# Performance work log

Measured on AMD Instinct MI355X. Metric: run time of the kernel, lower is better.

## Reference

```python
import jax, jax.numpy as jnp
import numpy as np

N, S, SKV, K, V = 16, 4096, 4096, 64, 64


def setup_inputs() -> dict:
    key = jax.random.key(0)
    k1, k2, k3, k4 = jax.random.split(key, 4)
    return {
        "queries": jax.random.normal(k1, (N, S, K), dtype=jnp.float32),
        "keys": jax.random.normal(k2, (N, SKV, K), dtype=jnp.float32),
        "values": jax.random.normal(k3, (N, SKV, V), dtype=jnp.float32),
        "mask": jax.random.normal(k4, (S, SKV), dtype=jnp.float32),
    }


def reference(queries, keys, values, mask):
    # queries scaled by K^{-1/2}, then baddbmm(mask, q, k^T)
    scale = queries.shape[-1] ** -0.5
    q = queries * scale
    # scores: [N, S, SKV]; mask (S, SKV) broadcasts over batch like baddbmm
    scores = jnp.einsum('nsk,ntk->nst', q, keys) + mask
    attn_weights = jax.nn.softmax(scores, axis=-1)
    # attn: [N, S, V]; dropout_p = 0.0 (eval), needs_weights = False
    attn = jnp.einsum('nst,ntv->nsv', attn_weights, values)
    return attn
```

## Files before the change

### kernel.cpp

```cpp
#include <hip/hip_runtime.h>
#include <cstdint>
#include <cstddef>


typedef __attribute__((ext_vector_type(8))) short short8;
typedef __attribute__((ext_vector_type(4))) short short4v;
typedef __attribute__((ext_vector_type(4))) float f32x4;
typedef __attribute__((ext_vector_type(4))) unsigned int uint4v;
typedef __attribute__((ext_vector_type(2))) unsigned int uint2v;

#define DEV __device__ __forceinline__

constexpr int N_B   = 16;
constexpr int S_Q   = 4096;
constexpr int S_KV  = 4096;
constexpr int DH    = 64;
constexpr int BQ    = 128;
constexpr int BK    = 64;
constexpr int ITERS = S_KV / BK;
constexpr int KSTR  = 72;
constexpr int VSTR  = 68;
constexpr int KIMG_B = 9216;
constexpr int VIMG_B = 9216;
constexpr int TILE_B = KIMG_B + VIMG_B;

#define LOG2E 1.44269504088896340736f
#define QSCALE (0.125f * 1.44269504088896340736f)

DEV unsigned short f2bf(float f) {
  union { float f; unsigned int i; } x; x.f = f;
  unsigned int r = x.i + 0x7FFFu + ((x.i >> 16) & 1u);
  return (unsigned short)(r >> 16);
}

#if __has_builtin(__builtin_amdgcn_cvt_pk_bf16_f32)
typedef __attribute__((ext_vector_type(2))) __bf16 bf16x2v;
DEV unsigned int packrne(float a, float b) {
  union { bf16x2v v; unsigned int u; } x;
  x.v = __builtin_amdgcn_cvt_pk_bf16_f32(a, b);
  return x.u;
}
#else
DEV unsigned int packrne(float a, float b) {
  union { float f; unsigned int u; } ua, ub; ua.f = a; ub.f = b;
  unsigned int ra = ua.u + 0x7FFFu + ((ua.u >> 16) & 1u);
  unsigned int rb = ub.u + 0x7FFFu + ((ub.u >> 16) & 1u);
  return __builtin_amdgcn_perm(rb, ra, 0x07060302u);
}
#endif

DEV f32x4 mfma16(short4v a, short4v b, f32x4 c) {
#if __has_builtin(__builtin_amdgcn_mfma_f32_16x16x16bf16_1k)
  return __builtin_amdgcn_mfma_f32_16x16x16bf16_1k(a, b, c, 0, 0, 0);
#elif __has_builtin(__builtin_amdgcn_mfma_f32_16x16x16_bf16)
  return __builtin_amdgcn_mfma_f32_16x16x16_bf16(a, b, c, 0, 0, 0);
#else
  asm volatile("v_mfma_f32_16x16x16_bf16 %0, %1, %2, %0\n\ts_nop 7\n\ts_nop 7"
               : "+v"(c) : "v"(a), "v"(b));
  return c;
#endif
}

DEV void stageK(unsigned short* buf, const f32x4* L, int tS) {
  const int r0 = tS >> 3, c = tS & 7;
  uint4v d0, d1;
  d0[0] = packrne(L[0][0], L[0][1]); d0[1] = packrne(L[0][2], L[0][3]);
  d0[2] = packrne(L[1][0], L[1][1]); d0[3] = packrne(L[1][2], L[1][3]);
  d1[0] = packrne(L[2][0], L[2][1]); d1[1] = packrne(L[2][2], L[2][3]);
  d1[2] = packrne(L[3][0], L[3][1]); d1[3] = packrne(L[3][2], L[3][3]);
  *(uint4v*)&buf[r0 * KSTR + c * 8]        = d0;
  *(uint4v*)&buf[(r0 + 32) * KSTR + c * 8] = d1;
}

DEV void stageV(unsigned short* buf, const f32x4* L, int tS) {
  const int a = tS >> 4;
  const int x = tS & 15;
  const int slot = (a + x) & 15;
#pragma unroll
  for (int j = 0; j < 4; ++j) {
    uint2v d;
    d[0] = packrne(L[0][j], L[1][j]);
    d[1] = packrne(L[2][j], L[3][j]);
    *(uint2v*)&buf[(x * 4 + j) * VSTR + slot * 4] = d;
  }
}

DEV void dma16(const void* g, void* l) {
#if __has_builtin(__builtin_amdgcn_global_load_lds)
  __builtin_amdgcn_global_load_lds(
      (const __attribute__((address_space(1))) unsigned int*)g,
      (__attribute__((address_space(3))) unsigned int*)l, 16, 0, 0);
#else
  ((uint4v*)l)[threadIdx.x & 63] = *(const uint4v*)g;
#endif
}

DEV void dmaTile(const char* gt, void* lk, void* lv, int w, int laneB) {
  if (w < 4) {
    const int base = w * 2048;
    dma16(gt + base + laneB,        (char*)lk + base);
    dma16(gt + base + 1024 + laneB, (char*)lk + base + 1024);
    if (w == 0) dma16(gt + 8192 + laneB, (char*)lk + 8192);
  } else {
    const char* g = gt + KIMG_B;
    const int base = (w - 4) * 2048;
    dma16(g + base + laneB,        (char*)lv + base);
    dma16(g + base + 1024 + laneB, (char*)lv + base + 1024);
    if (w == 4) dma16(g + 8192 + laneB, (char*)lv + 8192);
  }
}

__global__ __launch_bounds__(256)
void sdpa_prep(const float* __restrict__ Kg, const float* __restrict__ Vg,
               unsigned short* __restrict__ imgs) {
  const int b   = blockIdx.x;
  const int n   = b >> 6, tau = b & 63;
  const int tS  = threadIdx.x;
  unsigned short* img = imgs + (size_t)b * (TILE_B / 2);
  {
    const float* kp =
        Kg + ((size_t)n * S_KV + tau * 64 + (tS >> 3)) * DH + (tS & 7) * 8;
    f32x4 L[4];
    L[0] = *(const f32x4*)(kp);
    L[1] = *(const f32x4*)(kp + 4);
    L[2] = *(const f32x4*)(kp + 32 * DH);
    L[3] = *(const f32x4*)(kp + 32 * DH + 4);
    stageK(img, L, tS);
  }
  {
    const float* vp =
        Vg + ((size_t)n * S_KV + tau * 64 + (size_t)(tS >> 4) * 4) * DH
           + (tS & 15) * 4;
    f32x4 L[4];
#pragma unroll
    for (int i = 0; i < 4; ++i) L[i] = *(const f32x4*)(vp + i * DH);
    stageV(img + KIMG_B / 2, L, tS);
  }
}

template <int MW>
__global__ __launch_bounds__(512, MW)
void sdpa_fwd_dma(const float* __restrict__ Qg,
                  const float* __restrict__ Mg,
                  const unsigned short* __restrict__ imgs,
                  float* __restrict__ Ob,
                  float* __restrict__ Lb,
                  int nIter)
{
  __shared__ __align__(16) unsigned short ldsK[2][KIMG_B / 2];
  __shared__ __align__(16) unsigned short ldsV[2][VIMG_B / 2];

  const int n     = blockIdx.y;
  const int q0    = blockIdx.x * BQ;
  const int z     = blockIdx.z;
  const int t     = threadIdx.x;
  const int w     = t >> 6;
  const int lane  = t & 63;
  const int l15   = lane & 15;
  const int quad  = lane >> 4;
  const int qrow  = q0 + w * 16 + l15;
  const int laneB = lane * 16;
  const int tbase = n * 64 + z * nIter;

  short8 qf0, qf1;
  {
    const float* qp = Qg + ((size_t)n * S_Q + (size_t)qrow) * DH + quad * 8;
#pragma unroll
    for (int j = 0; j < 8; ++j) {
      qf0[j] = (short)f2bf(qp[j] * QSCALE);
      qf1[j] = (short)f2bf(qp[32 + j] * QSCALE);
    }
  }

  const float* mrow =
      Mg + (size_t)qrow * S_KV + (size_t)z * nIter * BK + quad * 4;

  f32x4 acc[4];
#pragma unroll
  for (int nt = 0; nt < 4; ++nt)
#pragma unroll
    for (int r = 0; r < 4; ++r) acc[nt][r] = 0.0f;
  float rs = 0.0f;

  dmaTile((const char*)imgs + (size_t)tbase * TILE_B,
          &ldsK[0][0], &ldsV[0][0], w, laneB);
  __syncthreads();

  for (int it = 0; it < nIter; ++it) {
    const int p   = it & 1;
    const int kv0 = it * BK;
    const bool more = (it + 1 < nIter);

    if (more)
      dmaTile((const char*)imgs + (size_t)(tbase + it + 1) * TILE_B,
              &ldsK[p ^ 1][0], &ldsV[p ^ 1][0], w, laneB);

    short4v pf[4];
#pragma unroll
    for (int h = 0; h < 4; ++h) {
      const short8 kf0 =
          *(const short8*)&ldsK[p][(l15 + 16 * h) * KSTR + quad * 8];
      const short8 kf1 =
          *(const short8*)&ldsK[p][(l15 + 16 * h) * KSTR + (quad + 4) * 8];
      const f32x4 mk = *(const f32x4*)(mrow + kv0 + 16 * h);
      f32x4 c = {0.f, 0.f, 0.f, 0.f};
      __builtin_amdgcn_s_setprio(1);
      c = __builtin_amdgcn_mfma_f32_16x16x32_bf16(kf0, qf0, c, 0, 0, 0);
      c = __builtin_amdgcn_mfma_f32_16x16x32_bf16(kf1, qf1, c, 0, 0, 0);
      __builtin_amdgcn_s_setprio(0);
      float e[4];
#pragma unroll
      for (int r = 0; r < 4; ++r)
        e[r] = __builtin_amdgcn_exp2f(fmaf(mk[r], LOG2E, c[r]));
      rs += (e[0] + e[1]) + (e[2] + e[3]);
      union { uint2v u; short4v s; } ue;
      ue.u[0] = packrne(e[0], e[1]);
      ue.u[1] = packrne(e[2], e[3]);
      pf[h] = ue.s;
    }

    __builtin_amdgcn_s_setprio(1);
#pragma unroll
    for (int nt = 0; nt < 4; ++nt) {
      const int vcol = l15 + 16 * nt;
      const int xr   = (l15 >> 2) + 4 * nt;
#pragma unroll
      for (int h = 0; h < 4; ++h) {
        const int slot = ((4 * h + quad) + xr) & 15;
        short4v vf = *(const short4v*)&ldsV[p][vcol * VSTR + slot * 4];
        acc[nt] = mfma16(vf, pf[h], acc[nt]);
      }
    }
    __builtin_amdgcn_s_setprio(0);

    __syncthreads();
  }

  rs += __shfl_xor(rs, 16, 64);
  rs += __shfl_xor(rs, 32, 64);

  if (Lb) {
    const size_t NSV = (size_t)N_B * S_Q * DH;
    float* ob = Ob + (size_t)z * NSV + ((size_t)n * S_Q + (size_t)qrow) * DH
              + quad * 4;
#pragma unroll
    for (int nt = 0; nt < 4; ++nt) *(f32x4*)(ob + 16 * nt) = acc[nt];
    if (quad == 0) {
      float* lp = Lb + (size_t)z * ((size_t)N_B * S_Q) + (size_t)n * S_Q
                + (size_t)qrow;
      lp[0] = rs;
    }
  } else {
    const float inv = 1.0f / rs;
    float* ob = Ob + ((size_t)n * S_Q + (size_t)qrow) * DH + quad * 4;
#pragma unroll
    for (int nt = 0; nt < 4; ++nt) {
      f32x4 o;
#pragma unroll
      for (int r = 0; r < 4; ++r) o[r] = acc[nt][r] * inv;
      *(f32x4*)(ob + 16 * nt) = o;
    }
  }
}

__global__ __launch_bounds__(512, 4)
void sdpa_fwd_reg(const float* __restrict__ Qg, const float* __restrict__ Kg,
                  const float* __restrict__ Vg, const float* __restrict__ Mg,
                  float* __restrict__ Og)
{
  __shared__ __align__(16) unsigned short ldsK[2][BK * KSTR];
  __shared__ __align__(16) unsigned short ldsV[2][DH * VSTR];

  const int n = blockIdx.y, q0 = blockIdx.x * BQ, t = threadIdx.x;
  const int w = t >> 6, lane = t & 63, l15 = lane & 15, quad = lane >> 4;
  const int qrow = q0 + w * 16 + l15;

  short8 qf0, qf1;
  {
    const float* qp = Qg + ((size_t)n * S_Q + (size_t)qrow) * DH + quad * 8;
#pragma unroll
    for (int j = 0; j < 8; ++j) {
      qf0[j] = (short)f2bf(qp[j] * QSCALE);
      qf1[j] = (short)f2bf(qp[32 + j] * QSCALE);
    }
  }
  const bool isK = (w < 4);
  const int  tS  = t & 255;
  const float* sgp =
      isK ? Kg + ((size_t)n * S_KV + (size_t)(tS >> 3)) * DH + (tS & 7) * 8
          : Vg + ((size_t)n * S_KV + (size_t)(tS >> 4) * 4) * DH + (tS & 15) * 4;
  const float* mrow = Mg + (size_t)qrow * S_KV + quad * 4;

  f32x4 acc[4];
#pragma unroll
  for (int nt = 0; nt < 4; ++nt)
#pragma unroll
    for (int r = 0; r < 4; ++r) acc[nt][r] = 0.0f;
  float rs = 0.0f;

  {
    f32x4 L[4];
    if (isK) {
      L[0] = *(const f32x4*)(sgp);
      L[1] = *(const f32x4*)(sgp + 4);
      L[2] = *(const f32x4*)(sgp + 32 * DH);
      L[3] = *(const f32x4*)(sgp + 32 * DH + 4);
      stageK(&ldsK[0][0], L, tS);
    } else {
#pragma unroll
      for (int i = 0; i < 4; ++i) L[i] = *(const f32x4*)(sgp + i * DH);
      stageV(&ldsV[0][0], L, tS);
    }
  }
  __syncthreads();

  for (int it = 0; it < ITERS; ++it) {
    const int p = it & 1, kv0 = it * BK;
    const bool more = (it + 1 < ITERS);
    short4v pf[4];
#pragma unroll
    for (int h = 0; h < 4; ++h) {
      const short8 kf0 =
          *(const short8*)&ldsK[p][(l15 + 16 * h) * KSTR + quad * 8];
      const short8 kf1 =
          *(const short8*)&ldsK[p][(l15 + 16 * h) * KSTR + (quad + 4) * 8];
      const f32x4 mk = *(const f32x4*)(mrow + kv0 + 16 * h);
      f32x4 c = {0.f, 0.f, 0.f, 0.f};
      c = __builtin_amdgcn_mfma_f32_16x16x32_bf16(kf0, qf0, c, 0, 0, 0);
      c = __builtin_amdgcn_mfma_f32_16x16x32_bf16(kf1, qf1, c, 0, 0, 0);
      float e[4];
#pragma unroll
      for (int r = 0; r < 4; ++r)
        e[r] = __builtin_amdgcn_exp2f(fmaf(mk[r], LOG2E, c[r]));
      rs += (e[0] + e[1]) + (e[2] + e[3]);
      union { uint2v u; short4v s; } ue;
      ue.u[0] = packrne(e[0], e[1]);
      ue.u[1] = packrne(e[2], e[3]);
      pf[h] = ue.s;
    }
    f32x4 L[4];
    if (more) {
      const float* np = sgp + (size_t)(kv0 + BK) * DH;
      if (isK) {
        L[0] = *(const f32x4*)(np);
        L[1] = *(const f32x4*)(np + 4);
        L[2] = *(const f32x4*)(np + 32 * DH);
        L[3] = *(const f32x4*)(np + 32 * DH + 4);
      } else {
#pragma unroll
        for (int i = 0; i < 4; ++i) L[i] = *(const f32x4*)(np + i * DH);
      }
    }
#pragma unroll
    for (int nt = 0; nt < 4; ++nt) {
      const int vcol = l15 + 16 * nt;
      const int xr   = (l15 >> 2) + 4 * nt;
#pragma unroll
      for (int h = 0; h < 4; ++h) {
        const int slot = ((4 * h + quad) + xr) & 15;
        short4v vf = *(const short4v*)&ldsV[p][vcol * VSTR + slot * 4];
        acc[nt] = mfma16(vf, pf[h], acc[nt]);
      }
    }
    if (more) {
      if (isK) stageK(&ldsK[p ^ 1][0], L, tS);
      else     stageV(&ldsV[p ^ 1][0], L, tS);
    }
    __syncthreads();
  }

  rs += __shfl_xor(rs, 16, 64);
  rs += __shfl_xor(rs, 32, 64);
  const float inv = 1.0f / rs;
  float* ob = Og + ((size_t)n * S_Q + (size_t)qrow) * DH + quad * 4;
#pragma unroll
  for (int nt = 0; nt < 4; ++nt) {
    f32x4 o;
#pragma unroll
    for (int r = 0; r < 4; ++r) o[r] = acc[nt][r] * inv;
    *(f32x4*)(ob + 16 * nt) = o;
  }
}

__global__ __launch_bounds__(256)
void sdpa_combine(const float* __restrict__ ws, float* __restrict__ Og) {
  constexpr size_t NSV = (size_t)N_B * S_Q * DH;
  constexpr size_t NS  = (size_t)N_B * S_Q;
  const size_t i = (size_t)blockIdx.x * 256 + threadIdx.x;
  const f32x4* A0 = (const f32x4*)ws;
  const f32x4* A1 = A0 + NSV / 4;
  const float* L0 = ws + 2 * NSV;
  const float* L1 = L0 + NS;
  const size_t qi = i >> 4;
  const f32x4 a = A0[i], b = A1[i];
  const float inv = 1.0f / (L0[qi] + L1[qi]);
  f32x4 o;
#pragma unroll
  for (int r = 0; r < 4; ++r) o[r] = (a[r] + b[r]) * inv;
  ((f32x4*)Og)[i] = o;
}

extern "C" void kernel_launch(void* const* d_in, const int* in_sizes, int n_in,
                              void* d_out, int out_size, void* d_ws, size_t ws_size,
                              hipStream_t stream) {
  (void)in_sizes; (void)n_in; (void)out_size;
  const float* q = (const float*)d_in[0];
  const float* k = (const float*)d_in[1];
  const float* v = (const float*)d_in[2];
  const float* m = (const float*)d_in[3];
  float* o = (float*)d_out;

  constexpr size_t NSV = (size_t)N_B * S_Q * DH;
  constexpr size_t NS  = (size_t)N_B * S_Q;
  constexpr size_t IMG_BYTES = (size_t)N_B * 64 * TILE_B;
  constexpr size_t SPL_BYTES = (2 * NSV + 2 * NS) * sizeof(float);

  static int use8 = -1;
  if (use8 < 0) {
    hipFuncAttributes attr{};
    use8 = 0;
    if (hipFuncGetAttributes(&attr,
            reinterpret_cast<const void*>(&sdpa_fwd_dma<8>)) == hipSuccess &&
        attr.localSizeBytes == 0)
      use8 = 1;
  }

  if (d_ws != nullptr && ws_size >= IMG_BYTES + SPL_BYTES && use8) {
    unsigned short* imgs = (unsigned short*)d_ws;
    float* part = (float*)((char*)d_ws + IMG_BYTES);
    hipLaunchKernelGGL(sdpa_prep, dim3(N_B * 64), dim3(256), 0, stream,
                       k, v, imgs);
    dim3 grid(S_Q / BQ, N_B, 2);
    hipLaunchKernelGGL((sdpa_fwd_dma<8>), grid, dim3(512), 0, stream,
                       q, m, imgs, part, part + 2 * NSV, ITERS / 2);
    hipLaunchKernelGGL(sdpa_combine, dim3((unsigned)(NSV / 4 / 256)),
                       dim3(256), 0, stream, (const float*)part, o);
  } else if (d_ws != nullptr && ws_size >= IMG_BYTES) {
    unsigned short* imgs = (unsigned short*)d_ws;
    hipLaunchKernelGGL(sdpa_prep, dim3(N_B * 64), dim3(256), 0, stream,
                       k, v, imgs);
    dim3 grid(S_Q / BQ, N_B, 1);
    hipLaunchKernelGGL((sdpa_fwd_dma<4>), grid, dim3(512), 0, stream,
                       q, m, imgs, o, (float*)nullptr, ITERS);
  } else {
    dim3 grid(S_Q / BQ, N_B);
    hipLaunchKernelGGL(sdpa_fwd_reg, grid, dim3(512), 0, stream,
                       q, k, v, m, o);
  }
}
```

Before: 295.7 us.

## Process two query tiles per wave and merge KV splits with atomics

Adds a dual-tile forward kernel in which each of 4 waves handles 32 query rows (two 16-row MFMA tiles), so every K and V fragment read from LDS is reused twice and the block shrinks to 256 threads. The two KV-split halves are now accumulated directly into the output and a row-sum buffer with float atomics, after a zero-fill kernel, and a normalize kernel runs last. This replaces the partial-result workspace and the combine kernel. In exchange it doubles register pressure per wave, issues many scalar global atomics, and adds a zeroing pass over the output.

New measurement: 296.6 us. About the same (+0.3%).

```diff
diff --git a/kernel.cpp b/kernel.cpp
--- a/kernel.cpp
+++ b/kernel.cpp
@@ -107,6 +107,17 @@
     dma16(g + base + laneB,        (char*)lv + base);
     dma16(g + base + 1024 + laneB, (char*)lv + base + 1024);
     if (w == 4) dma16(g + 8192 + laneB, (char*)lv + 8192);
+  }
+}
+
+DEV void dmaTile4(const char* gt, char* lk, char* lv, int w, int laneB) {
+#pragma unroll
+  for (int i = 0; i < 5; ++i) {
+    const int c = w + 4 * i;
+    if (c < 18) {
+      if (c < 9) dma16(gt + c * 1024 + laneB, lk + c * 1024);
+      else dma16(gt + KIMG_B + (c - 9) * 1024 + laneB, lv + (c - 9) * 1024);
+    }
   }
 }
 
@@ -139,13 +150,13 @@
 }
 
 template <int MW>
-__global__ __launch_bounds__(512, MW)
-void sdpa_fwd_dma(const float* __restrict__ Qg,
-                  const float* __restrict__ Mg,
-                  const unsigned short* __restrict__ imgs,
-                  float* __restrict__ Ob,
-                  float* __restrict__ Lb,
-                  int nIter)
+__global__ __launch_bounds__(256, MW)
+void sdpa_fwd_dual(const float* __restrict__ Qg,
+                   const float* __restrict__ Mg,
+                   const unsigned short* __restrict__ imgs,
+                   float* __restrict__ Og,
+                   float* __restrict__ Lbuf,
+                   int nIter)
 {
   __shared__ __align__(16) unsigned short ldsK[2][KIMG_B / 2];
   __shared__ __align__(16) unsigned short ldsV[2][VIMG_B / 2];
@@ -158,9 +169,153 @@
   const int lane  = t & 63;
   const int l15   = lane & 15;
   const int quad  = lane >> 4;
+  const int qA    = q0 + w * 32 + l15;
+  const int laneB = lane * 16;
+  const int tbase = n * 64 + z * nIter;
+
+  short8 qfA0, qfA1, qfB0, qfB1;
+  {
+    const float* qp = Qg + ((size_t)n * S_Q + (size_t)qA) * DH + quad * 8;
+#pragma unroll
+    for (int j = 0; j < 8; ++j) {
+      qfA0[j] = (short)f2bf(qp[j] * QSCALE);
+      qfA1[j] = (short)f2bf(qp[32 + j] * QSCALE);
+      qfB0[j] = (short)f2bf(qp[16 * DH + j] * QSCALE);
+      qfB1[j] = (short)f2bf(qp[16 * DH + 32 + j] * QSCALE);
+    }
+  }
+
+  const float* mrowA =
+      Mg + (size_t)qA * S_KV + (size_t)z * nIter * BK + quad * 4;
+  const float* mrowB = mrowA + (size_t)16 * S_KV;
+
+  f32x4 accA[4], accB[4];
+#pragma unroll
+  for (int nt = 0; nt < 4; ++nt)
+#pragma unroll
+    for (int r = 0; r < 4; ++r) { accA[nt][r] = 0.0f; accB[nt][r] = 0.0f; }
+  float rsA = 0.0f, rsB = 0.0f;
+
+  dmaTile4((const char*)imgs + (size_t)tbase * TILE_B,
+           (char*)&ldsK[0][0], (char*)&ldsV[0][0], w, laneB);
+  __syncthreads();
+
+  for (int it = 0; it < nIter; ++it) {
+    const int p   = it & 1;
+    const int kv0 = it * BK;
+    const bool more = (it + 1 < nIter);
+
+    if (more)
+      dmaTile4((const char*)imgs + (size_t)(tbase + it + 1) * TILE_B,
+               (char*)&ldsK[p ^ 1][0], (char*)&ldsV[p ^ 1][0], w, laneB);
+
+    short4v pfA[4], pfB[4];
+#pragma unroll
+    for (int h = 0; h < 4; ++h) {
+      const short8 kf0 =
+          *(const short8*)&ldsK[p][(l15 + 16 * h) * KSTR + quad * 8];
+      const short8 kf1 =
+          *(const short8*)&ldsK[p][(l15 + 16 * h) * KSTR + (quad + 4) * 8];
+      const f32x4 mkA = *(const f32x4*)(mrowA + kv0 + 16 * h);
+      const f32x4 mkB = *(const f32x4*)(mrowB + kv0 + 16 * h);
+      f32x4 cA = {0.f, 0.f, 0.f, 0.f}, cB = {0.f, 0.f, 0.f, 0.f};
+      __builtin_amdgcn_s_setprio(1);
+      cA = __builtin_amdgcn_mfma_f32_16x16x32_bf16(kf0, qfA0, cA, 0, 0, 0);
+      cB = __builtin_amdgcn_mfma_f32_16x16x32_bf16(kf0, qfB0, cB, 0, 0, 0);
+      cA = __builtin_amdgcn_mfma_f32_16x16x32_bf16(kf1, qfA1, cA, 0, 0, 0);
+      cB = __builtin_amdgcn_mfma_f32_16x16x32_bf16(kf1, qfB1, cB, 0, 0, 0);
+      __builtin_amdgcn_s_setprio(0);
+      float eA[4], eB[4];
+#pragma unroll
+      for (int r = 0; r < 4; ++r) {
+        eA[r] = __builtin_amdgcn_exp2f(fmaf(mkA[r], LOG2E, cA[r]));
+        eB[r] = __builtin_amdgcn_exp2f(fmaf(mkB[r], LOG2E, cB[r]));
+      }
+      rsA += (eA[0] + eA[1]) + (eA[2] + eA[3]);
+      rsB += (eB[0] + eB[1]) + (eB[2] + eB[3]);
+      union { uint2v u; short4v s; } ua, ub;
+      ua.u[0] = packrne(eA[0], eA[1]); ua.u[1] = packrne(eA[2], eA[3]);
+      ub.u[0] = packrne(eB[0], eB[1]); ub.u[1] = packrne(eB[2], eB[3]);
+      pfA[h] = ua.s; pfB[h] = ub.s;
+    }
+
+    __builtin_amdgcn_s_setprio(1);
+#pragma unroll
+    for (int nt = 0; nt < 4; ++nt) {
+      const int vcol = l15 + 16 * nt;
+      const int xr   = (l15 >> 2) + 4 * nt;
+#pragma unroll
+      for (int h = 0; h < 4; ++h) {
+        const int slot = ((4 * h + quad) + xr) & 15;
+        short4v vf = *(const short4v*)&ldsV[p][vcol * VSTR + slot * 4];
+        accA[nt] = mfma16(vf, pfA[h], accA[nt]);
+        accB[nt] = mfma16(vf, pfB[h], accB[nt]);
+      }
+    }
+    __builtin_amdgcn_s_setprio(0);
+
+    __syncthreads();
+  }
+
+  rsA += __shfl_xor(rsA, 16, 64);
+  rsA += __shfl_xor(rsA, 32, 64);
+  rsB += __shfl_xor(rsB, 16, 64);
+  rsB += __shfl_xor(rsB, 32, 64);
+  if (quad == 0) {
+    atomicAdd(&Lbuf[(size_t)n * S_Q + qA],      rsA);
+    atomicAdd(&Lbuf[(size_t)n * S_Q + qA + 16], rsB);
+  }
+  float* obA = Og + ((size_t)n * S_Q + (size_t)qA) * DH + quad * 4;
+  float* obB = obA + (size_t)16 * DH;
+#pragma unroll
+  for (int nt = 0; nt < 4; ++nt)
+#pragma unroll
+    for (int r = 0; r < 4; ++r) {
+      atomicAdd(obA + 16 * nt + r, accA[nt][r]);
+      atomicAdd(obB + 16 * nt + r, accB[nt][r]);
+    }
+}
+
+__global__ __launch_bounds__(256)
+void sdpa_zero(float* __restrict__ Og, float* __restrict__ Lbuf) {
+  constexpr size_t NS = (size_t)N_B * S_Q;
+  const size_t i = (size_t)blockIdx.x * 256 + threadIdx.x;
+  const f32x4 zz = {0.f, 0.f, 0.f, 0.f};
+  ((f32x4*)Og)[i] = zz;
+  if (i < NS / 4) ((f32x4*)Lbuf)[i] = zz;
+}
+
+__global__ __launch_bounds__(256)
+void sdpa_norm(float* __restrict__ Og, const float* __restrict__ Lbuf) {
+  const size_t i = (size_t)blockIdx.x * 256 + threadIdx.x;
+  const size_t qi = i >> 4;
+  f32x4 v = ((f32x4*)Og)[i];
+  const float inv = 1.0f / Lbuf[qi];
+#pragma unroll
+  for (int r = 0; r < 4; ++r) v[r] *= inv;
+  ((f32x4*)Og)[i] = v;
+}
+
+template <int MW>
+__global__ __launch_bounds__(512, MW)
+void sdpa_fwd_dma(const float* __restrict__ Qg,
+                  const float* __restrict__ Mg,
+                  const unsigned short* __restrict__ imgs,
+                  float* __restrict__ Og, int nIter)
+{
+  __shared__ __align__(16) unsigned short ldsK[2][KIMG_B / 2];
+  __shared__ __align__(16) unsigned short ldsV[2][VIMG_B / 2];
+
+  const int n     = blockIdx.y;
+  const int q0    = blockIdx.x * BQ;
+  const int t     = threadIdx.x;
+  const int w     = t >> 6;
+  const int lane  = t & 63;
+  const int l15   = lane & 15;
+  const int quad  = lane >> 4;
   const int qrow  = q0 + w * 16 + l15;
   const int laneB = lane * 16;
-  const int tbase = n * 64 + z * nIter;
+  const int tbase = n * 64;
 
   short8 qf0, qf1;
   {
@@ -171,9 +326,7 @@
       qf1[j] = (short)f2bf(qp[32 + j] * QSCALE);
     }
   }
-
-  const float* mrow =
-      Mg + (size_t)qrow * S_KV + (size_t)z * nIter * BK + quad * 4;
+  const float* mrow = Mg + (size_t)qrow * S_KV + quad * 4;
 
   f32x4 acc[4];
 #pragma unroll
@@ -238,28 +391,14 @@
 
   rs += __shfl_xor(rs, 16, 64);
   rs += __shfl_xor(rs, 32, 64);
-
-  if (Lb) {
-    const size_t NSV = (size_t)N_B * S_Q * DH;
-    float* ob = Ob + (size_t)z * NSV + ((size_t)n * S_Q + (size_t)qrow) * DH
-              + quad * 4;
-#pragma unroll
-    for (int nt = 0; nt < 4; ++nt) *(f32x4*)(ob + 16 * nt) = acc[nt];
-    if (quad == 0) {
-      float* lp = Lb + (size_t)z * ((size_t)N_B * S_Q) + (size_t)n * S_Q
-                + (size_t)qrow;
-      lp[0] = rs;
-    }
-  } else {
-    const float inv = 1.0f / rs;
-    float* ob = Ob + ((size_t)n * S_Q + (size_t)qrow) * DH + quad * 4;
-#pragma unroll
-    for (int nt = 0; nt < 4; ++nt) {
-      f32x4 o;
-#pragma unroll
-      for (int r = 0; r < 4; ++r) o[r] = acc[nt][r] * inv;
-      *(f32x4*)(ob + 16 * nt) = o;
-    }
+  const float inv = 1.0f / rs;
+  float* ob = Og + ((size_t)n * S_Q + (size_t)qrow) * DH + quad * 4;
+#pragma unroll
+  for (int nt = 0; nt < 4; ++nt) {
+    f32x4 o;
+#pragma unroll
+    for (int r = 0; r < 4; ++r) o[r] = acc[nt][r] * inv;
+    *(f32x4*)(ob + 16 * nt) = o;
   }
 }
 
@@ -382,24 +521,6 @@
   }
 }
 
-__global__ __launch_bounds__(256)
-void sdpa_combine(const float* __restrict__ ws, float* __restrict__ Og) {
-  constexpr size_t NSV = (size_t)N_B * S_Q * DH;
-  constexpr size_t NS  = (size_t)N_B * S_Q;
-  const size_t i = (size_t)blockIdx.x * 256 + threadIdx.x;
-  const f32x4* A0 = (const f32x4*)ws;
-  const f32x4* A1 = A0 + NSV / 4;
-  const float* L0 = ws + 2 * NSV;
-  const float* L1 = L0 + NS;
-  const size_t qi = i >> 4;
-  const f32x4 a = A0[i], b = A1[i];
-  const float inv = 1.0f / (L0[qi] + L1[qi]);
-  f32x4 o;
-#pragma unroll
-  for (int r = 0; r < 4; ++r) o[r] = (a[r] + b[r]) * inv;
-  ((f32x4*)Og)[i] = o;
-}
-
 extern "C" void kernel_launch(void* const* d_in, const int* in_sizes, int n_in,
                               void* d_out, int out_size, void* d_ws, size_t ws_size,
                               hipStream_t stream) {
@@ -413,35 +534,37 @@
   constexpr size_t NSV = (size_t)N_B * S_Q * DH;
   constexpr size_t NS  = (size_t)N_B * S_Q;
   constexpr size_t IMG_BYTES = (size_t)N_B * 64 * TILE_B;
-  constexpr size_t SPL_BYTES = (2 * NSV + 2 * NS) * sizeof(float);
-
-  static int use8 = -1;
-  if (use8 < 0) {
+  constexpr size_t DUAL_NEED = IMG_BYTES + NS * sizeof(float);
+
+  static int useDual = -1;
+  if (useDual < 0) {
     hipFuncAttributes attr{};
-    use8 = 0;
+    useDual = 0;
     if (hipFuncGetAttributes(&attr,
-            reinterpret_cast<const void*>(&sdpa_fwd_dma<8>)) == hipSuccess &&
+            reinterpret_cast<const void*>(&sdpa_fwd_dual<4>)) == hipSuccess &&
         attr.localSizeBytes == 0)
-      use8 = 1;
-  }
-
-  if (d_ws != nullptr && ws_size >= IMG_BYTES + SPL_BYTES && use8) {
+      useDual = 1;
+  }
+
+  if (d_ws != nullptr && ws_size >= DUAL_NEED && useDual) {
     unsigned short* imgs = (unsigned short*)d_ws;
-    float* part = (float*)((char*)d_ws + IMG_BYTES);
+    float* lbuf = (float*)((char*)d_ws + IMG_BYTES);
     hipLaunchKernelGGL(sdpa_prep, dim3(N_B * 64), dim3(256), 0, stream,
                        k, v, imgs);
+    hipLaunchKernelGGL(sdpa_zero, dim3((unsigned)(NSV / 4 / 256)), dim3(256),
+                       0, stream, o, lbuf);
     dim3 grid(S_Q / BQ, N_B, 2);
-    hipLaunchKernelGGL((sdpa_fwd_dma<8>), grid, dim3(512), 0, stream,
-                       q, m, imgs, part, part + 2 * NSV, ITERS / 2);
-    hipLaunchKernelGGL(sdpa_combine, dim3((unsigned)(NSV / 4 / 256)),
-                       dim3(256), 0, stream, (const float*)part, o);
+    hipLaunchKernelGGL((sdpa_fwd_dual<4>), grid, dim3(256), 0, stream,
+                       q, m, imgs, o, lbuf, ITERS / 2);
+    hipLaunchKernelGGL(sdpa_norm, dim3((unsigned)(NSV / 4 / 256)), dim3(256),
+                       0, stream, o, (const float*)lbuf);
   } else if (d_ws != nullptr && ws_size >= IMG_BYTES) {
     unsigned short* imgs = (unsigned short*)d_ws;
     hipLaunchKernelGGL(sdpa_prep, dim3(N_B * 64), dim3(256), 0, stream,
                        k, v, imgs);
     dim3 grid(S_Q / BQ, N_B, 1);
     hipLaunchKernelGGL((sdpa_fwd_dma<4>), grid, dim3(512), 0, stream,
-                       q, m, imgs, o, (float*)nullptr, ITERS);
+                       q, m, imgs, o, ITERS);
   } else {
     dim3 grid(S_Q / BQ, N_B);
     hipLaunchKernelGGL(sdpa_fwd_reg, grid, dim3(512), 0, stream,
```

## Swizzle K tile in LDS without padding and add atomic split-KV fallback

Applied to the files above, without the earlier changes.

K rows in LDS are now stored unpadded at 64 elements, with an XOR swizzle on the 16-byte column chunk, replacing the 72-element padded stride. This shrinks the K image and drops the extra DMA issue for the padding tail, while aiming to keep the reads free of bank conflicts. A new mid-workspace path zeroes the output, accumulates both KV halves with atomics, then normalizes in a separate kernel. The default path (enough workspace) still uses the two-buffer combine, so mostly the swizzle and smaller tile apply there.

New measurement: 288.4 us. -2.5%, faster.

```diff
diff --git a/kernel.cpp b/kernel.cpp
--- a/kernel.cpp
+++ b/kernel.cpp
@@ -18,9 +18,9 @@
 constexpr int BQ    = 128;
 constexpr int BK    = 64;
 constexpr int ITERS = S_KV / BK;
-constexpr int KSTR  = 72;
+constexpr int KROW  = 64;
 constexpr int VSTR  = 68;
-constexpr int KIMG_B = 9216;
+constexpr int KIMG_B = 8192;
 constexpr int VIMG_B = 9216;
 constexpr int TILE_B = KIMG_B + VIMG_B;
 
@@ -63,13 +63,14 @@
 
 DEV void stageK(unsigned short* buf, const f32x4* L, int tS) {
   const int r0 = tS >> 3, c = tS & 7;
+  const int cs = (c ^ (r0 & 7)) * 8;
   uint4v d0, d1;
   d0[0] = packrne(L[0][0], L[0][1]); d0[1] = packrne(L[0][2], L[0][3]);
   d0[2] = packrne(L[1][0], L[1][1]); d0[3] = packrne(L[1][2], L[1][3]);
   d1[0] = packrne(L[2][0], L[2][1]); d1[1] = packrne(L[2][2], L[2][3]);
   d1[2] = packrne(L[3][0], L[3][1]); d1[3] = packrne(L[3][2], L[3][3]);
-  *(uint4v*)&buf[r0 * KSTR + c * 8]        = d0;
-  *(uint4v*)&buf[(r0 + 32) * KSTR + c * 8] = d1;
+  *(uint4v*)&buf[r0 * KROW + cs]        = d0;
+  *(uint4v*)&buf[(r0 + 32) * KROW + cs] = d1;
 }
 
 DEV void stageV(unsigned short* buf, const f32x4* L, int tS) {
@@ -100,7 +101,6 @@
     const int base = w * 2048;
     dma16(gt + base + laneB,        (char*)lk + base);
     dma16(gt + base + 1024 + laneB, (char*)lk + base + 1024);
-    if (w == 0) dma16(gt + 8192 + laneB, (char*)lk + 8192);
   } else {
     const char* g = gt + KIMG_B;
     const int base = (w - 4) * 2048;
@@ -145,7 +145,7 @@
                   const unsigned short* __restrict__ imgs,
                   float* __restrict__ Ob,
                   float* __restrict__ Lb,
-                  int nIter)
+                  int nIter, int mode)
 {
   __shared__ __align__(16) unsigned short ldsK[2][KIMG_B / 2];
   __shared__ __align__(16) unsigned short ldsV[2][VIMG_B / 2];
@@ -175,6 +175,10 @@
   const float* mrow =
       Mg + (size_t)qrow * S_KV + (size_t)z * nIter * BK + quad * 4;
 
+  const int swz = l15 & 7;
+  const int c0 = (quad ^ swz) * 8;
+  const int c1 = ((quad + 4) ^ swz) * 8;
+
   f32x4 acc[4];
 #pragma unroll
   for (int nt = 0; nt < 4; ++nt)
@@ -195,13 +199,13 @@
       dmaTile((const char*)imgs + (size_t)(tbase + it + 1) * TILE_B,
               &ldsK[p ^ 1][0], &ldsV[p ^ 1][0], w, laneB);
 
+    const unsigned short* kb = &ldsK[p][l15 * KROW];
+
     short4v pf[4];
 #pragma unroll
     for (int h = 0; h < 4; ++h) {
-      const short8 kf0 =
-          *(const short8*)&ldsK[p][(l15 + 16 * h) * KSTR + quad * 8];
-      const short8 kf1 =
-          *(const short8*)&ldsK[p][(l15 + 16 * h) * KSTR + (quad + 4) * 8];
+      const short8 kf0 = *(const short8*)(kb + h * 1024 + c0);
+      const short8 kf1 = *(const short8*)(kb + h * 1024 + c1);
       const f32x4 mk = *(const f32x4*)(mrow + kv0 + 16 * h);
       f32x4 c = {0.f, 0.f, 0.f, 0.f};
       __builtin_amdgcn_s_setprio(1);
@@ -239,147 +243,53 @@
   rs += __shfl_xor(rs, 16, 64);
   rs += __shfl_xor(rs, 32, 64);
 
-  if (Lb) {
+  if (mode == 0) {
+    const float inv = 1.0f / rs;
+    float* ob = Ob + ((size_t)n * S_Q + (size_t)qrow) * DH + quad * 4;
+#pragma unroll
+    for (int nt = 0; nt < 4; ++nt) {
+      f32x4 o;
+#pragma unroll
+      for (int r = 0; r < 4; ++r) o[r] = acc[nt][r] * inv;
+      *(f32x4*)(ob + 16 * nt) = o;
+    }
+  } else if (mode == 1) {
     const size_t NSV = (size_t)N_B * S_Q * DH;
     float* ob = Ob + (size_t)z * NSV + ((size_t)n * S_Q + (size_t)qrow) * DH
               + quad * 4;
 #pragma unroll
     for (int nt = 0; nt < 4; ++nt) *(f32x4*)(ob + 16 * nt) = acc[nt];
-    if (quad == 0) {
-      float* lp = Lb + (size_t)z * ((size_t)N_B * S_Q) + (size_t)n * S_Q
-                + (size_t)qrow;
-      lp[0] = rs;
-    }
+    if (quad == 0)
+      Lb[(size_t)z * ((size_t)N_B * S_Q) + (size_t)n * S_Q + qrow] = rs;
   } else {
-    const float inv = 1.0f / rs;
     float* ob = Ob + ((size_t)n * S_Q + (size_t)qrow) * DH + quad * 4;
 #pragma unroll
-    for (int nt = 0; nt < 4; ++nt) {
-      f32x4 o;
-#pragma unroll
-      for (int r = 0; r < 4; ++r) o[r] = acc[nt][r] * inv;
-      *(f32x4*)(ob + 16 * nt) = o;
-    }
-  }
-}
-
-__global__ __launch_bounds__(512, 4)
-void sdpa_fwd_reg(const float* __restrict__ Qg, const float* __restrict__ Kg,
-                  const float* __restrict__ Vg, const float* __restrict__ Mg,
-                  float* __restrict__ Og)
-{
-  __shared__ __align__(16) unsigned short ldsK[2][BK * KSTR];
-  __shared__ __align__(16) unsigned short ldsV[2][DH * VSTR];
-
-  const int n = blockIdx.y, q0 = blockIdx.x * BQ, t = threadIdx.x;
-  const int w = t >> 6, lane = t & 63, l15 = lane & 15, quad = lane >> 4;
-  const int qrow = q0 + w * 16 + l15;
-
-  short8 qf0, qf1;
-  {
-    const float* qp = Qg + ((size_t)n * S_Q + (size_t)qrow) * DH + quad * 8;
-#pragma unroll
-    for (int j = 0; j < 8; ++j) {
-      qf0[j] = (short)f2bf(qp[j] * QSCALE);
-      qf1[j] = (short)f2bf(qp[32 + j] * QSCALE);
-    }
-  }
-  const bool isK = (w < 4);
-  const int  tS  = t & 255;
-  const float* sgp =
-      isK ? Kg + ((size_t)n * S_KV + (size_t)(tS >> 3)) * DH + (tS & 7) * 8
-          : Vg + ((size_t)n * S_KV + (size_t)(tS >> 4) * 4) * DH + (tS & 15) * 4;
-  const float* mrow = Mg + (size_t)qrow * S_KV + quad * 4;
-
-  f32x4 acc[4];
-#pragma unroll
-  for (int nt = 0; nt < 4; ++nt)
-#pragma unroll
-    for (int r = 0; r < 4; ++r) acc[nt][r] = 0.0f;
-  float rs = 0.0f;
-
-  {
-    f32x4 L[4];
-    if (isK) {
-      L[0] = *(const f32x4*)(sgp);
-      L[1] = *(const f32x4*)(sgp + 4);
-      L[2] = *(const f32x4*)(sgp + 32 * DH);
-      L[3] = *(const f32x4*)(sgp + 32 * DH + 4);
-      stageK(&ldsK[0][0], L, tS);
-    } else {
-#pragma unroll
-      for (int i = 0; i < 4; ++i) L[i] = *(const f32x4*)(sgp + i * DH);
-      stageV(&ldsV[0][0], L, tS);
-    }
-  }
-  __syncthreads();
-
-  for (int it = 0; it < ITERS; ++it) {
-    const int p = it & 1, kv0 = it * BK;
-    const bool more = (it + 1 < ITERS);
-    short4v pf[4];
-#pragma unroll
-    for (int h = 0; h < 4; ++h) {
-      const short8 kf0 =
-          *(const short8*)&ldsK[p][(l15 + 16 * h) * KSTR + quad * 8];
-      const short8 kf1 =
-          *(const short8*)&ldsK[p][(l15 + 16 * h) * KSTR + (quad + 4) * 8];
-      const f32x4 mk = *(const f32x4*)(mrow + kv0 + 16 * h);
-      f32x4 c = {0.f, 0.f, 0.f, 0.f};
-      c = __builtin_amdgcn_mfma_f32_16x16x32_bf16(kf0, qf0, c, 0, 0, 0);
-      c = __builtin_amdgcn_mfma_f32_16x16x32_bf16(kf1, qf1, c, 0, 0, 0);
-      float e[4];
+    for (int nt = 0; nt < 4; ++nt)
 #pragma unroll
       for (int r = 0; r < 4; ++r)
-        e[r] = __builtin_amdgcn_exp2f(fmaf(mk[r], LOG2E, c[r]));
-      rs += (e[0] + e[1]) + (e[2] + e[3]);
-      union { uint2v u; short4v s; } ue;
-      ue.u[0] = packrne(e[0], e[1]);
-      ue.u[1] = packrne(e[2], e[3]);
-      pf[h] = ue.s;
-    }
-    f32x4 L[4];
-    if (more) {
-      const float* np = sgp + (size_t)(kv0 + BK) * DH;
-      if (isK) {
-        L[0] = *(const f32x4*)(np);
-        L[1] = *(const f32x4*)(np + 4);
-        L[2] = *(const f32x4*)(np + 32 * DH);
-        L[3] = *(const f32x4*)(np + 32 * DH + 4);
-      } else {
-#pragma unroll
-        for (int i = 0; i < 4; ++i) L[i] = *(const f32x4*)(np + i * DH);
-      }
-    }
-#pragma unroll
-    for (int nt = 0; nt < 4; ++nt) {
-      const int vcol = l15 + 16 * nt;
-      const int xr   = (l15 >> 2) + 4 * nt;
-#pragma unroll
-      for (int h = 0; h < 4; ++h) {
-        const int slot = ((4 * h + quad) + xr) & 15;
-        short4v vf = *(const short4v*)&ldsV[p][vcol * VSTR + slot * 4];
-        acc[nt] = mfma16(vf, pf[h], acc[nt]);
-      }
-    }
-    if (more) {
-      if (isK) stageK(&ldsK[p ^ 1][0], L, tS);
-      else     stageV(&ldsV[p ^ 1][0], L, tS);
-    }
-    __syncthreads();
-  }
-
-  rs += __shfl_xor(rs, 16, 64);
-  rs += __shfl_xor(rs, 32, 64);
-  const float inv = 1.0f / rs;
-  float* ob = Og + ((size_t)n * S_Q + (size_t)qrow) * DH + quad * 4;
-#pragma unroll
-  for (int nt = 0; nt < 4; ++nt) {
-    f32x4 o;
-#pragma unroll
-    for (int r = 0; r < 4; ++r) o[r] = acc[nt][r] * inv;
-    *(f32x4*)(ob + 16 * nt) = o;
-  }
+        atomicAdd(ob + 16 * nt + r, acc[nt][r]);
+    if (quad == 0) atomicAdd(&Lb[(size_t)n * S_Q + qrow], rs);
+  }
+}
+
+__global__ __launch_bounds__(256)
+void sdpa_zero(float* __restrict__ Og, float* __restrict__ Lbuf) {
+  constexpr size_t NS = (size_t)N_B * S_Q;
+  const size_t i = (size_t)blockIdx.x * 256 + threadIdx.x;
+  const f32x4 zz = {0.f, 0.f, 0.f, 0.f};
+  ((f32x4*)Og)[i] = zz;
+  if (i < NS / 4) ((f32x4*)Lbuf)[i] = zz;
+}
+
+__global__ __launch_bounds__(256)
+void sdpa_norm(float* __restrict__ Og, const float* __restrict__ Lbuf) {
+  const size_t i = (size_t)blockIdx.x * 256 + threadIdx.x;
+  const size_t qi = i >> 4;
+  f32x4 v = ((f32x4*)Og)[i];
+  const float inv = 1.0f / Lbuf[qi];
+#pragma unroll
+  for (int r = 0; r < 4; ++r) v[r] *= inv;
+  ((f32x4*)Og)[i] = v;
 }
 
 __global__ __launch_bounds__(256)
@@ -400,6 +310,128 @@
   ((f32x4*)Og)[i] = o;
 }
 
+__global__ __launch_bounds__(512, 4)
+void sdpa_fwd_reg(const float* __restrict__ Qg, const float* __restrict__ Kg,
+                  const float* __restrict__ Vg, const float* __restrict__ Mg,
+                  float* __restrict__ Og)
+{
+  __shared__ __align__(16) unsigned short ldsK[2][KIMG_B / 2];
+  __shared__ __align__(16) unsigned short ldsV[2][VIMG_B / 2];
+
+  const int n = blockIdx.y, q0 = blockIdx.x * BQ, t = threadIdx.x;
+  const int w = t >> 6, lane = t & 63, l15 = lane & 15, quad = lane >> 4;
+  const int qrow = q0 + w * 16 + l15;
+
+  short8 qf0, qf1;
+  {
+    const float* qp = Qg + ((size_t)n * S_Q + (size_t)qrow) * DH + quad * 8;
+#pragma unroll
+    for (int j = 0; j < 8; ++j) {
+      qf0[j] = (short)f2bf(qp[j] * QSCALE);
+      qf1[j] = (short)f2bf(qp[32 + j] * QSCALE);
+    }
+  }
+  const bool isK = (w < 4);
+  const int  tS  = t & 255;
+  const float* sgp =
+      isK ? Kg + ((size_t)n * S_KV + (size_t)(tS >> 3)) * DH + (tS & 7) * 8
+          : Vg + ((size_t)n * S_KV + (size_t)(tS >> 4) * 4) * DH + (tS & 15) * 4;
+  const float* mrow = Mg + (size_t)qrow * S_KV + quad * 4;
+
+  const int swz = l15 & 7;
+  const int c0 = (quad ^ swz) * 8;
+  const int c1 = ((quad + 4) ^ swz) * 8;
+
+  f32x4 acc[4];
+#pragma unroll
+  for (int nt = 0; nt < 4; ++nt)
+#pragma unroll
+    for (int r = 0; r < 4; ++r) acc[nt][r] = 0.0f;
+  float rs = 0.0f;
+
+  {
+    f32x4 L[4];
+    if (isK) {
+      L[0] = *(const f32x4*)(sgp);
+      L[1] = *(const f32x4*)(sgp + 4);
+      L[2] = *(const f32x4*)(sgp + 32 * DH);
+      L[3] = *(const f32x4*)(sgp + 32 * DH + 4);
+      stageK(&ldsK[0][0], L, tS);
+    } else {
+#pragma unroll
+      for (int i = 0; i < 4; ++i) L[i] = *(const f32x4*)(sgp + i * DH);
+      stageV(&ldsV[0][0], L, tS);
+    }
+  }
+  __syncthreads();
+
+  for (int it = 0; it < ITERS; ++it) {
+    const int p = it & 1, kv0 = it * BK;
+    const bool more = (it + 1 < ITERS);
+    const unsigned short* kb = &ldsK[p][l15 * KROW];
+    short4v pf[4];
+#pragma unroll
+    for (int h = 0; h < 4; ++h) {
+      const short8 kf0 = *(const short8*)(kb + h * 1024 + c0);
+      const short8 kf1 = *(const short8*)(kb + h * 1024 + c1);
+      const f32x4 mk = *(const f32x4*)(mrow + kv0 + 16 * h);
+      f32x4 c = {0.f, 0.f, 0.f, 0.f};
+      c = __builtin_amdgcn_mfma_f32_16x16x32_bf16(kf0, qf0, c, 0, 0, 0);
+      c = __builtin_amdgcn_mfma_f32_16x16x32_bf16(kf1, qf1, c, 0, 0, 0);
+      float e[4];
+#pragma unroll
+      for (int r = 0; r < 4; ++r)
+        e[r] = __builtin_amdgcn_exp2f(fmaf(mk[r], LOG2E, c[r]));
+      rs += (e[0] + e[1]) + (e[2] + e[3]);
+      union { uint2v u; short4v s; } ue;
+      ue.u[0] = packrne(e[0], e[1]);
+      ue.u[1] = packrne(e[2], e[3]);
+      pf[h] = ue.s;
+    }
+    f32x4 L[4];
+    if (more) {
+      const float* np = sgp + (size_t)(kv0 + BK) * DH;
+      if (isK) {
+        L[0] = *(const f32x4*)(np);
+        L[1] = *(const f32x4*)(np + 4);
+        L[2] = *(const f32x4*)(np + 32 * DH);
+        L[3] = *(const f32x4*)(np + 32 * DH + 4);
+      } else {
+#pragma unroll
+        for (int i = 0; i < 4; ++i) L[i] = *(const f32x4*)(np + i * DH);
+      }
+    }
+#pragma unroll
+    for (int nt = 0; nt < 4; ++nt) {
+      const int vcol = l15 + 16 * nt;
+      const int xr   = (l15 >> 2) + 4 * nt;
+#pragma unroll
+      for (int h = 0; h < 4; ++h) {
+        const int slot = ((4 * h + quad) + xr) & 15;
+        short4v vf = *(const short4v*)&ldsV[p][vcol * VSTR + slot * 4];
+        acc[nt] = mfma16(vf, pf[h], acc[nt]);
+      }
+    }
+    if (more) {
+      if (isK) stageK(&ldsK[p ^ 1][0], L, tS);
+      else     stageV(&ldsV[p ^ 1][0], L, tS);
+    }
+    __syncthreads();
+  }
+
+  rs += __shfl_xor(rs, 16, 64);
+  rs += __shfl_xor(rs, 32, 64);
+  const float inv = 1.0f / rs;
+  float* ob = Og + ((size_t)n * S_Q + (size_t)qrow) * DH + quad * 4;
+#pragma unroll
+  for (int nt = 0; nt < 4; ++nt) {
+    f32x4 o;
+#pragma unroll
+    for (int r = 0; r < 4; ++r) o[r] = acc[nt][r] * inv;
+    *(f32x4*)(ob + 16 * nt) = o;
+  }
+}
+
 extern "C" void kernel_launch(void* const* d_in, const int* in_sizes, int n_in,
                               void* d_out, int out_size, void* d_ws, size_t ws_size,
                               hipStream_t stream) {
@@ -413,7 +445,7 @@
   constexpr size_t NSV = (size_t)N_B * S_Q * DH;
   constexpr size_t NS  = (size_t)N_B * S_Q;
   constexpr size_t IMG_BYTES = (size_t)N_B * 64 * TILE_B;
-  constexpr size_t SPL_BYTES = (2 * NSV + 2 * NS) * sizeof(float);
+  constexpr size_t PART_BYTES = (2 * NSV + 2 * NS) * sizeof(float);
 
   static int use8 = -1;
   if (use8 < 0) {
@@ -425,23 +457,36 @@
       use8 = 1;
   }
 
-  if (d_ws != nullptr && ws_size >= IMG_BYTES + SPL_BYTES && use8) {
+  if (use8 && d_ws != nullptr && ws_size >= IMG_BYTES + PART_BYTES) {
     unsigned short* imgs = (unsigned short*)d_ws;
     float* part = (float*)((char*)d_ws + IMG_BYTES);
     hipLaunchKernelGGL(sdpa_prep, dim3(N_B * 64), dim3(256), 0, stream,
                        k, v, imgs);
     dim3 grid(S_Q / BQ, N_B, 2);
     hipLaunchKernelGGL((sdpa_fwd_dma<8>), grid, dim3(512), 0, stream,
-                       q, m, imgs, part, part + 2 * NSV, ITERS / 2);
+                       q, m, imgs, part, part + 2 * NSV, ITERS / 2, 1);
     hipLaunchKernelGGL(sdpa_combine, dim3((unsigned)(NSV / 4 / 256)),
                        dim3(256), 0, stream, (const float*)part, o);
+  } else if (use8 && d_ws != nullptr &&
+             ws_size >= IMG_BYTES + NS * sizeof(float)) {
+    unsigned short* imgs = (unsigned short*)d_ws;
+    float* lbuf = (float*)((char*)d_ws + IMG_BYTES);
+    hipLaunchKernelGGL(sdpa_prep, dim3(N_B * 64), dim3(256), 0, stream,
+                       k, v, imgs);
+    hipLaunchKernelGGL(sdpa_zero, dim3((unsigned)(NSV / 4 / 256)), dim3(256),
+                       0, stream, o, lbuf);
+    dim3 grid(S_Q / BQ, N_B, 2);
+    hipLaunchKernelGGL((sdpa_fwd_dma<8>), grid, dim3(512), 0, stream,
+                       q, m, imgs, o, lbuf, ITERS / 2, 2);
+    hipLaunchKernelGGL(sdpa_norm, dim3((unsigned)(NSV / 4 / 256)), dim3(256),
+                       0, stream, o, (const float*)lbuf);
   } else if (d_ws != nullptr && ws_size >= IMG_BYTES) {
     unsigned short* imgs = (unsigned short*)d_ws;
     hipLaunchKernelGGL(sdpa_prep, dim3(N_B * 64), dim3(256), 0, stream,
                        k, v, imgs);
     dim3 grid(S_Q / BQ, N_B, 1);
     hipLaunchKernelGGL((sdpa_fwd_dma<4>), grid, dim3(512), 0, stream,
-                       q, m, imgs, o, (float*)nullptr, ITERS);
+                       q, m, imgs, o, (float*)nullptr, ITERS, 0);
   } else {
     dim3 grid(S_Q / BQ, N_B);
     hipLaunchKernelGGL(sdpa_fwd_reg, grid, dim3(512), 0, stream,
```

## Replace split-KV 512-thread kernel with 4-wave 64-row blocks and XOR-swizzled K layout

Applied to the files above, without the earlier changes.

Drops the two-way KV split and its combine pass, and runs a single kernel with 256-thread blocks, each handling 64 query rows over the full KV range. Four blocks are targeted per CU. The K tile in LDS is now unpadded with an XOR swizzle on 16-byte chunks, which avoids bank conflicts while shrinking the image, and the DMA loader is adapted so four waves move both K and V. This removes the partial-result write/read traffic and the extra launch, at the cost of more blocks that each reload the full K/V stream, so staged-tile reuse across query rows is halved.

New measurement: 291.9 us. About the same (-1.3%).

```diff
diff --git a/kernel.cpp b/kernel.cpp
--- a/kernel.cpp
+++ b/kernel.cpp
@@ -15,12 +15,12 @@
 constexpr int S_Q   = 4096;
 constexpr int S_KV  = 4096;
 constexpr int DH    = 64;
-constexpr int BQ    = 128;
+constexpr int BQ    = 64;
 constexpr int BK    = 64;
 constexpr int ITERS = S_KV / BK;
-constexpr int KSTR  = 72;
+constexpr int KROW  = 64;
 constexpr int VSTR  = 68;
-constexpr int KIMG_B = 9216;
+constexpr int KIMG_B = 8192;
 constexpr int VIMG_B = 9216;
 constexpr int TILE_B = KIMG_B + VIMG_B;
 
@@ -63,13 +63,14 @@
 
 DEV void stageK(unsigned short* buf, const f32x4* L, int tS) {
   const int r0 = tS >> 3, c = tS & 7;
+  const int cs = (c ^ (r0 & 7)) * 8;
   uint4v d0, d1;
   d0[0] = packrne(L[0][0], L[0][1]); d0[1] = packrne(L[0][2], L[0][3]);
   d0[2] = packrne(L[1][0], L[1][1]); d0[3] = packrne(L[1][2], L[1][3]);
   d1[0] = packrne(L[2][0], L[2][1]); d1[1] = packrne(L[2][2], L[2][3]);
   d1[2] = packrne(L[3][0], L[3][1]); d1[3] = packrne(L[3][2], L[3][3]);
-  *(uint4v*)&buf[r0 * KSTR + c * 8]        = d0;
-  *(uint4v*)&buf[(r0 + 32) * KSTR + c * 8] = d1;
+  *(uint4v*)&buf[r0 * KROW + cs]        = d0;
+  *(uint4v*)&buf[(r0 + 32) * KROW + cs] = d1;
 }
 
 DEV void stageV(unsigned short* buf, const f32x4* L, int tS) {
@@ -95,19 +96,14 @@
 #endif
 }
 
-DEV void dmaTile(const char* gt, void* lk, void* lv, int w, int laneB) {
-  if (w < 4) {
-    const int base = w * 2048;
-    dma16(gt + base + laneB,        (char*)lk + base);
-    dma16(gt + base + 1024 + laneB, (char*)lk + base + 1024);
-    if (w == 0) dma16(gt + 8192 + laneB, (char*)lk + 8192);
-  } else {
-    const char* g = gt + KIMG_B;
-    const int base = (w - 4) * 2048;
-    dma16(g + base + laneB,        (char*)lv + base);
-    dma16(g + base + 1024 + laneB, (char*)lv + base + 1024);
-    if (w == 4) dma16(g + 8192 + laneB, (char*)lv + 8192);
-  }
+DEV void dmaTile4w(const char* gt, char* lk, char* lv, int w, int laneB) {
+  const int b0 = w * 1024;
+  dma16(gt + b0 + laneB,        lk + b0);
+  dma16(gt + b0 + 4096 + laneB, lk + b0 + 4096);
+  const char* gv = gt + KIMG_B;
+  dma16(gv + b0 + laneB,        lv + b0);
+  dma16(gv + b0 + 4096 + laneB, lv + b0 + 4096);
+  if (w == 0) dma16(gv + 8192 + laneB, lv + 8192);
 }
 
 __global__ __launch_bounds__(256)
@@ -138,21 +134,17 @@
   }
 }
 
-template <int MW>
-__global__ __launch_bounds__(512, MW)
-void sdpa_fwd_dma(const float* __restrict__ Qg,
-                  const float* __restrict__ Mg,
-                  const unsigned short* __restrict__ imgs,
-                  float* __restrict__ Ob,
-                  float* __restrict__ Lb,
-                  int nIter)
+__global__ __launch_bounds__(256, 4)
+void sdpa_fwd4(const float* __restrict__ Qg,
+               const float* __restrict__ Mg,
+               const unsigned short* __restrict__ imgs,
+               float* __restrict__ Og)
 {
   __shared__ __align__(16) unsigned short ldsK[2][KIMG_B / 2];
   __shared__ __align__(16) unsigned short ldsV[2][VIMG_B / 2];
 
   const int n     = blockIdx.y;
   const int q0    = blockIdx.x * BQ;
-  const int z     = blockIdx.z;
   const int t     = threadIdx.x;
   const int w     = t >> 6;
   const int lane  = t & 63;
@@ -160,7 +152,7 @@
   const int quad  = lane >> 4;
   const int qrow  = q0 + w * 16 + l15;
   const int laneB = lane * 16;
-  const int tbase = n * 64 + z * nIter;
+  const int tbase = n * 64;
 
   short8 qf0, qf1;
   {
@@ -172,8 +164,11 @@
     }
   }
 
-  const float* mrow =
-      Mg + (size_t)qrow * S_KV + (size_t)z * nIter * BK + quad * 4;
+  const float* mrow = Mg + (size_t)qrow * S_KV + quad * 4;
+
+  const int swz = l15 & 7;
+  const int c0 = (quad ^ swz) * 8;
+  const int c1 = ((quad + 4) ^ swz) * 8;
 
   f32x4 acc[4];
 #pragma unroll
@@ -182,26 +177,26 @@
     for (int r = 0; r < 4; ++r) acc[nt][r] = 0.0f;
   float rs = 0.0f;
 
-  dmaTile((const char*)imgs + (size_t)tbase * TILE_B,
-          &ldsK[0][0], &ldsV[0][0], w, laneB);
+  dmaTile4w((const char*)imgs + (size_t)tbase * TILE_B,
+            (char*)&ldsK[0][0], (char*)&ldsV[0][0], w, laneB);
   __syncthreads();
 
-  for (int it = 0; it < nIter; ++it) {
+  for (int it = 0; it < ITERS; ++it) {
     const int p   = it & 1;
     const int kv0 = it * BK;
-    const bool more = (it + 1 < nIter);
+    const bool more = (it + 1 < ITERS);
 
     if (more)
-      dmaTile((const char*)imgs + (size_t)(tbase + it + 1) * TILE_B,
-              &ldsK[p ^ 1][0], &ldsV[p ^ 1][0], w, laneB);
+      dmaTile4w((const char*)imgs + (size_t)(tbase + it + 1) * TILE_B,
+                (char*)&ldsK[p ^ 1][0], (char*)&ldsV[p ^ 1][0], w, laneB);
+
+    const unsigned short* kb = &ldsK[p][l15 * KROW];
 
     short4v pf[4];
 #pragma unroll
     for (int h = 0; h < 4; ++h) {
-      const short8 kf0 =
-          *(const short8*)&ldsK[p][(l15 + 16 * h) * KSTR + quad * 8];
-      const short8 kf1 =
-          *(const short8*)&ldsK[p][(l15 + 16 * h) * KSTR + (quad + 4) * 8];
+      const short8 kf0 = *(const short8*)(kb + h * 1024 + c0);
+      const short8 kf1 = *(const short8*)(kb + h * 1024 + c1);
       const f32x4 mk = *(const f32x4*)(mrow + kv0 + 16 * h);
       f32x4 c = {0.f, 0.f, 0.f, 0.f};
       __builtin_amdgcn_s_setprio(1);
@@ -238,28 +233,14 @@
 
   rs += __shfl_xor(rs, 16, 64);
   rs += __shfl_xor(rs, 32, 64);
-
-  if (Lb) {
-    const size_t NSV = (size_t)N_B * S_Q * DH;
-    float* ob = Ob + (size_t)z * NSV + ((size_t)n * S_Q + (size_t)qrow) * DH
-              + quad * 4;
-#pragma unroll
-    for (int nt = 0; nt < 4; ++nt) *(f32x4*)(ob + 16 * nt) = acc[nt];
-    if (quad == 0) {
-      float* lp = Lb + (size_t)z * ((size_t)N_B * S_Q) + (size_t)n * S_Q
-                + (size_t)qrow;
-      lp[0] = rs;
-    }
-  } else {
-    const float inv = 1.0f / rs;
-    float* ob = Ob + ((size_t)n * S_Q + (size_t)qrow) * DH + quad * 4;
-#pragma unroll
-    for (int nt = 0; nt < 4; ++nt) {
-      f32x4 o;
-#pragma unroll
-      for (int r = 0; r < 4; ++r) o[r] = acc[nt][r] * inv;
-      *(f32x4*)(ob + 16 * nt) = o;
-    }
+  const float inv = 1.0f / rs;
+  float* ob = Og + ((size_t)n * S_Q + (size_t)qrow) * DH + quad * 4;
+#pragma unroll
+  for (int nt = 0; nt < 4; ++nt) {
+    f32x4 o;
+#pragma unroll
+    for (int r = 0; r < 4; ++r) o[r] = acc[nt][r] * inv;
+    *(f32x4*)(ob + 16 * nt) = o;
   }
 }
 
@@ -268,10 +249,10 @@
                   const float* __restrict__ Vg, const float* __restrict__ Mg,
                   float* __restrict__ Og)
 {
-  __shared__ __align__(16) unsigned short ldsK[2][BK * KSTR];
-  __shared__ __align__(16) unsigned short ldsV[2][DH * VSTR];
-
-  const int n = blockIdx.y, q0 = blockIdx.x * BQ, t = threadIdx.x;
+  __shared__ __align__(16) unsigned short ldsK[2][KIMG_B / 2];
+  __shared__ __align__(16) unsigned short ldsV[2][VIMG_B / 2];
+
+  const int n = blockIdx.y, q0 = blockIdx.x * 128, t = threadIdx.x;
   const int w = t >> 6, lane = t & 63, l15 = lane & 15, quad = lane >> 4;
   const int qrow = q0 + w * 16 + l15;
 
@@ -290,6 +271,10 @@
       isK ? Kg + ((size_t)n * S_KV + (size_t)(tS >> 3)) * DH + (tS & 7) * 8
           : Vg + ((size_t)n * S_KV + (size_t)(tS >> 4) * 4) * DH + (tS & 15) * 4;
   const float* mrow = Mg + (size_t)qrow * S_KV + quad * 4;
+
+  const int swz = l15 & 7;
+  const int c0 = (quad ^ swz) * 8;
+  const int c1 = ((quad + 4) ^ swz) * 8;
 
   f32x4 acc[4];
 #pragma unroll
@@ -317,13 +302,12 @@
   for (int it = 0; it < ITERS; ++it) {
     const int p = it & 1, kv0 = it * BK;
     const bool more = (it + 1 < ITERS);
+    const unsigned short* kb = &ldsK[p][l15 * KROW];
     short4v pf[4];
 #pragma unroll
     for (int h = 0; h < 4; ++h) {
-      const short8 kf0 =
-          *(const short8*)&ldsK[p][(l15 + 16 * h) * KSTR + quad * 8];
-      const short8 kf1 =
-          *(const short8*)&ldsK[p][(l15 + 16 * h) * KSTR + (quad + 4) * 8];
+      const short8 kf0 = *(const short8*)(kb + h * 1024 + c0);
+      const short8 kf1 = *(const short8*)(kb + h * 1024 + c1);
       const f32x4 mk = *(const f32x4*)(mrow + kv0 + 16 * h);
       f32x4 c = {0.f, 0.f, 0.f, 0.f};
       c = __builtin_amdgcn_mfma_f32_16x16x32_bf16(kf0, qf0, c, 0, 0, 0);
@@ -382,24 +366,6 @@
   }
 }
 
-__global__ __launch_bounds__(256)
-void sdpa_combine(const float* __restrict__ ws, float* __restrict__ Og) {
-  constexpr size_t NSV = (size_t)N_B * S_Q * DH;
-  constexpr size_t NS  = (size_t)N_B * S_Q;
-  const size_t i = (size_t)blockIdx.x * 256 + threadIdx.x;
-  const f32x4* A0 = (const f32x4*)ws;
-  const f32x4* A1 = A0 + NSV / 4;
-  const float* L0 = ws + 2 * NSV;
-  const float* L1 = L0 + NS;
-  const size_t qi = i >> 4;
-  const f32x4 a = A0[i], b = A1[i];
-  const float inv = 1.0f / (L0[qi] + L1[qi]);
-  f32x4 o;
-#pragma unroll
-  for (int r = 0; r < 4; ++r) o[r] = (a[r] + b[r]) * inv;
-  ((f32x4*)Og)[i] = o;
-}
-
 extern "C" void kernel_launch(void* const* d_in, const int* in_sizes, int n_in,
                               void* d_out, int out_size, void* d_ws, size_t ws_size,
                               hipStream_t stream) {
@@ -410,40 +376,17 @@
   const float* m = (const float*)d_in[3];
   float* o = (float*)d_out;
 
-  constexpr size_t NSV = (size_t)N_B * S_Q * DH;
-  constexpr size_t NS  = (size_t)N_B * S_Q;
   constexpr size_t IMG_BYTES = (size_t)N_B * 64 * TILE_B;
-  constexpr size_t SPL_BYTES = (2 * NSV + 2 * NS) * sizeof(float);
-
-  static int use8 = -1;
-  if (use8 < 0) {
-    hipFuncAttributes attr{};
-    use8 = 0;
-    if (hipFuncGetAttributes(&attr,
-            reinterpret_cast<const void*>(&sdpa_fwd_dma<8>)) == hipSuccess &&
-        attr.localSizeBytes == 0)
-      use8 = 1;
-  }
-
-  if (d_ws != nullptr && ws_size >= IMG_BYTES + SPL_BYTES && use8) {
-    unsigned short* imgs = (unsigned short*)d_ws;
-    float* part = (float*)((char*)d_ws + IMG_BYTES);
-    hipLaunchKernelGGL(sdpa_prep, dim3(N_B * 64), dim3(256), 0, stream,
-                       k, v, imgs);
-    dim3 grid(S_Q / BQ, N_B, 2);
-    hipLaunchKernelGGL((sdpa_fwd_dma<8>), grid, dim3(512), 0, stream,
-                       q, m, imgs, part, part + 2 * NSV, ITERS / 2);
-    hipLaunchKernelGGL(sdpa_combine, dim3((unsigned)(NSV / 4 / 256)),
-                       dim3(256), 0, stream, (const float*)part, o);
-  } else if (d_ws != nullptr && ws_size >= IMG_BYTES) {
+
+  if (d_ws != nullptr && ws_size >= IMG_BYTES) {
     unsigned short* imgs = (unsigned short*)d_ws;
     hipLaunchKernelGGL(sdpa_prep, dim3(N_B * 64), dim3(256), 0, stream,
                        k, v, imgs);
-    dim3 grid(S_Q / BQ, N_B, 1);
-    hipLaunchKernelGGL((sdpa_fwd_dma<4>), grid, dim3(512), 0, stream,
-                       q, m, imgs, o, (float*)nullptr, ITERS);
+    dim3 grid(S_Q / BQ, N_B);
+    hipLaunchKernelGGL(sdpa_fwd4, grid, dim3(256), 0, stream,
+                       q, m, imgs, o);
   } else {
-    dim3 grid(S_Q / BQ, N_B);
+    dim3 grid(S_Q / 128, N_B);
     hipLaunchKernelGGL(sdpa_fwd_reg, grid, dim3(512), 0, stream,
                        q, k, v, m, o);
   }
```
